# Kernel tuning notes

Hardware: AMD Instinct MI355X
Metric: run time of the kernel (lower is better)

The kernel has to match this reference:

```python
import jax, jax.numpy as jnp
import numpy as np

N_ATOMS = 8_000_000
N_REC = 2_000_000
N_POC = 500_000
N_CHAINS = 4


def setup_inputs() -> dict:
    key = jax.random.key(0)
    k1, k2, k3, k4 = jax.random.split(key, 4)
    # coordinates in nm, inside a ~5 nm box
    positions = jax.random.uniform(k1, (N_ATOMS, 3), dtype=jnp.float32) * 5.0
    box_vectors = jnp.diag(jnp.array([5.0, 5.0, 5.0], dtype=jnp.float32))
    # unique receptor atom indices into positions
    rec_indices = jax.random.permutation(k2, N_ATOMS)[:N_REC].astype(jnp.int32)
    # unique pocket indices INTO THE REC ARRAY (poc_pos = rec_pos[poc_indices])
    poc_indices = jax.random.permutation(k3, N_REC)[:N_POC].astype(jnp.int32)
    # contiguous chain assignment over rec atoms, all chains present in pocket
    chain_ids = ((jnp.arange(N_REC, dtype=jnp.int32) * N_CHAINS) // N_REC).astype(jnp.int32)
    poc_chain_ids = chain_ids[poc_indices]
    ref_poc = jax.random.uniform(k4, (N_POC, 3), dtype=jnp.float32) * 5.0
    k = jnp.float32(100.0)  # kJ/mol/nm^2
    return {
        "positions": positions, "box_vectors": box_vectors, "ref_poc": ref_poc,
        "k": k, "rec_indices": rec_indices, "poc_indices": poc_indices,
        "chain_ids": chain_ids, "poc_chain_ids": poc_chain_ids, "n_chains": N_CHAINS,
    }


def best_periodic_translation(pos1, pos2, box_vectors):
    # pos1, pos2: [C,3]; box_vectors: [3,3] (rows are lattice vectors)
    delta = pos2 - pos1
    inv = 1.0 / jnp.diag(box_vectors)
    s3 = jnp.round(delta[:, 2] * inv[2])
    delta = delta - s3[:, None] * box_vectors[2]
    s2 = jnp.round(delta[:, 1] * inv[1])
    delta = delta - s2[:, None] * box_vectors[1]
    s1 = jnp.round(delta[:, 0] * inv[0])
    return s1[:, None] * box_vectors[0] + s2[:, None] * box_vectors[1] + s3[:, None] * box_vectors[2]


def reference(positions, box_vectors, ref_poc, k, rec_indices, poc_indices, chain_ids, poc_chain_ids, n_chains):
    rec_pos = positions[rec_indices]  # [R,3]
    # Per-chain pocket COM. NOTE: original indexes global positions here
    # (positions[poc_chain_indices]), NOT rec_pos -- reproduced faithfully.
    poc_glob = positions[poc_indices]  # [P,3]
    counts = jax.ops.segment_sum(jnp.ones((poc_glob.shape[0],), poc_glob.dtype), poc_chain_ids, num_segments=n_chains)  # [C]
    poc_com = jax.ops.segment_sum(poc_glob, poc_chain_ids, num_segments=n_chains) / counts[:, None]  # [C,3]
    ref_com = jax.ops.segment_sum(ref_poc, poc_chain_ids, num_segments=n_chains) / counts[:, None]  # [C,3]
    best_t = best_periodic_translation(poc_com, ref_com, box_vectors)  # [C,3]
    rec_pos = rec_pos + best_t[chain_ids]  # translate each chain into the reference image

    poc_pos = rec_pos[poc_indices]  # [P,3]
    rec_origin = jnp.mean(rec_pos, axis=0)
    rec_centered = rec_pos - rec_origin
    r_sq = jnp.sum(rec_centered ** 2, axis=1)  # [R]
    F = jnp.zeros_like(rec_pos).at[poc_indices].set(-2.0 * k * (poc_pos - ref_poc))
    F_mean = jnp.mean(F, axis=0)
    torque = jnp.cross(rec_centered, F)
    torque_mean = jnp.mean(torque, axis=0)
    F_rot = jnp.cross(torque_mean[None], rec_centered) / r_sq[:, None]
    F_final = jnp.zeros_like(positions).at[rec_indices].set(F_mean + F_rot)
    return (jnp.float32(0.0), F_final)
```

## Files before the change

### kernel.cpp

```cpp
#include <hip/hip_runtime.h>


typedef unsigned int uint32;
typedef unsigned char uchar;

#define MAXC 16
#define W_BT 0
#define W_O 48
#define W_FM 52
#define W_TM 56
#define W_ACC 64

#define GCOUNT_OFF 4096
#define REC_OFF 8192
#define NB 512
#define BSH 14
#define BUCKET_ATOMS (1 << BSH)
#define CAP 5120
#define INV8_OFF (REC_OFF + NB * CAP * 4)

#define K1_KPT 16
#define K1_CHUNK (256 * K1_KPT)

__device__ inline float waveSum(float v) {
#pragma unroll
  for (int off = 32; off > 0; off >>= 1) v += __shfl_down(v, off, 64);
  return v;
}

__global__ __launch_bounds__(256) void k_part_pocket(
    const float* __restrict__ pos, const float* __restrict__ ref_poc,
    const int* __restrict__ rec_idx, const int* __restrict__ cid,
    const int* __restrict__ poc_idx, const int* __restrict__ poc_cid,
    const int* __restrict__ ncp, int R, int P,
    uint32* __restrict__ gcount, uint32* __restrict__ grecords,
    float* __restrict__ ws) {
  const int tid = threadIdx.x;
  const int C = ncp[0];
  const int gsz = gridDim.x * blockDim.x;

  if (C <= 4) {
    float vals[43];
#pragma unroll
    for (int v = 0; v < 43; ++v) vals[v] = 0.f;
    for (int r = blockIdx.x * blockDim.x + tid; r < P; r += gsz) {
      int i2 = poc_idx[r];
      int c2 = poc_cid[r];
      int ri = rec_idx[i2];
      float gx = pos[3 * i2 + 0], gy = pos[3 * i2 + 1], gz = pos[3 * i2 + 2];
      float px = pos[3 * ri + 0], py = pos[3 * ri + 1], pz = pos[3 * ri + 2];
      float rx = ref_poc[3 * r + 0], ry = ref_poc[3 * r + 1], rz = ref_poc[3 * r + 2];
      vals[0] += py * rz - pz * ry;
      vals[1] += pz * rx - px * rz;
      vals[2] += px * ry - py * rx;
#pragma unroll
      for (int cc = 0; cc < 4; ++cc) {
        bool m = (c2 == cc);
        float* a = &vals[3 + cc * 10];
        a[0] += m ? gx : 0.f;  a[1] += m ? gy : 0.f;  a[2] += m ? gz : 0.f;
        a[3] += m ? rx : 0.f;  a[4] += m ? ry : 0.f;  a[5] += m ? rz : 0.f;
        a[6] += m ? px : 0.f;  a[7] += m ? py : 0.f;  a[8] += m ? pz : 0.f;
        a[9] += m ? 1.f : 0.f;
      }
    }
    __shared__ float red[4][43];
    const int wid = tid >> 6;
#pragma unroll
    for (int v = 0; v < 43; ++v) {
      float s = waveSum(vals[v]);
      if ((tid & 63) == 0) red[wid][v] = s;
    }
    __syncthreads();
    for (int t = tid; t < 43; t += 256)
      atomicAdd(&ws[W_ACC + 19 + t],
                red[0][t] + red[1][t] + red[2][t] + red[3][t]);
    __syncthreads();
  } else {
    __shared__ float accL[3 + MAXC * 10];
    for (int t = tid; t < 3 + MAXC * 10; t += 256) accL[t] = 0.f;
    __syncthreads();
    for (int r = blockIdx.x * blockDim.x + tid; r < P; r += gsz) {
      int i2 = poc_idx[r];
      int c2 = poc_cid[r];
      int ri = rec_idx[i2];
      float gx = pos[3 * i2 + 0], gy = pos[3 * i2 + 1], gz = pos[3 * i2 + 2];
      float px = pos[3 * ri + 0], py = pos[3 * ri + 1], pz = pos[3 * ri + 2];
      float rx = ref_poc[3 * r + 0], ry = ref_poc[3 * r + 1], rz = ref_poc[3 * r + 2];
      atomicAdd(&accL[0], py * rz - pz * ry);
      atomicAdd(&accL[1], pz * rx - px * rz);
      atomicAdd(&accL[2], px * ry - py * rx);
      float* a = &accL[3 + c2 * 10];
      atomicAdd(&a[0], gx); atomicAdd(&a[1], gy); atomicAdd(&a[2], gz);
      atomicAdd(&a[3], rx); atomicAdd(&a[4], ry); atomicAdd(&a[5], rz);
      atomicAdd(&a[6], px); atomicAdd(&a[7], py); atomicAdd(&a[8], pz);
      atomicAdd(&a[9], 1.f);
    }
    __syncthreads();
    for (int t = tid; t < 3 + MAXC * 10; t += 256)
      if (accL[t] != 0.f) atomicAdd(&ws[W_ACC + 19 + t], accL[t]);
    __syncthreads();
  }

  __shared__ uint32 hist[NB], curs[NB], base[NB];
  for (int r0 = blockIdx.x * K1_CHUNK; r0 < R; r0 += gridDim.x * K1_CHUNK) {
    int cnt = R - r0; if (cnt > K1_CHUNK) cnt = K1_CHUNK;
    for (int t = tid; t < NB; t += 256) { hist[t] = 0u; curs[t] = 0u; }
    __syncthreads();
    uint32 enc[K1_KPT];
#pragma unroll
    for (int j = 0; j < K1_KPT; ++j) {
      int t = tid + j * 256;
      uint32 e = 0xFFFFFFFFu;
      if (t < cnt) {
        uint32 idx = (uint32)rec_idx[r0 + t];
        uint32 c = (uint32)cid[r0 + t] & 255u;
        e = (idx << 8) | c;
        atomicAdd(&hist[idx >> BSH], 1u);
      }
      enc[j] = e;
    }
    __syncthreads();
    for (int t = tid; t < NB; t += 256) {
      uint32 h = hist[t];
      base[t] = h ? atomicAdd(&gcount[t], h) : 0u;
    }
    __syncthreads();
#pragma unroll
    for (int j = 0; j < K1_KPT; ++j) {
      uint32 e = enc[j];
      if (e != 0xFFFFFFFFu) {
        uint32 b = e >> (8 + BSH);
        uint32 slot = base[b] + atomicAdd(&curs[b], 1u);
        if (slot < CAP) grecords[b * CAP + slot] = e;
      }
    }
    __syncthreads();
  }
}

__global__ __launch_bounds__(256) void k_bucket_build(
    const float4* __restrict__ pos4, const int* __restrict__ ncp,
    const uint32* __restrict__ gcount, const uint32* __restrict__ grecords,
    int N, uchar* __restrict__ inv8, float* __restrict__ ws) {
  const int tid = threadIdx.x;
  const int b = blockIdx.x;
  const int a0 = b << BSH;
  if (a0 >= N) return;
  int natoms = N - a0; if (natoms > BUCKET_ATOMS) natoms = BUCKET_ATOMS;

  __shared__ uchar map_[BUCKET_ATOMS];
  __shared__ float cnt16[MAXC];
  uint4* m16 = (uint4*)map_;
  uint4 ff; ff.x = ff.y = ff.z = ff.w = 0xFFFFFFFFu;
  for (int t = tid; t < BUCKET_ATOMS / 16; t += 256) m16[t] = ff;
  const int C = ncp[0];
  if (C > 4) for (int t = tid; t < MAXC; t += 256) cnt16[t] = 0.f;
  __syncthreads();

  int n = (int)gcount[b]; if (n > CAP) n = CAP;
  float c0 = 0.f, c1 = 0.f, c2 = 0.f, c3 = 0.f;
  for (int t = tid; t < n; t += 256) {
    uint32 e = grecords[b * CAP + t];
    uint32 ia = (e >> 8) & (BUCKET_ATOMS - 1);
    uint32 c = e & 255u;
    map_[ia] = (uchar)c;
    if (C <= 4) {
      c0 += (c == 0u) ? 1.f : 0.f;
      c1 += (c == 1u) ? 1.f : 0.f;
      c2 += (c == 2u) ? 1.f : 0.f;
      c3 += (c == 3u) ? 1.f : 0.f;
    } else {
      atomicAdd(&cnt16[c], 1.f);
    }
  }
  __syncthreads();

  uchar* dst = inv8 + a0;
  if (natoms == BUCKET_ATOMS) {
    uint4* d16 = (uint4*)dst;
    for (int t = tid; t < BUCKET_ATOMS / 16; t += 256) d16[t] = m16[t];
  } else {
    for (int t = tid; t < natoms; t += 256) dst[t] = map_[t];
  }

  float sx = 0.f, sy = 0.f, sz = 0.f;
  int ngf = natoms >> 2;
  const uchar4* m4 = (const uchar4*)map_;
  int g0 = a0 >> 2;
  for (int g = tid; g < ngf; g += 256) {
    float4 p0 = pos4[3 * (g0 + g) + 0];
    float4 p1 = pos4[3 * (g0 + g) + 1];
    float4 p2 = pos4[3 * (g0 + g) + 2];
    uchar4 m = m4[g];
    if (m.x != 255) { sx += p0.x; sy += p0.y; sz += p0.z; }
    if (m.y != 255) { sx += p0.w; sy += p1.x; sz += p1.y; }
    if (m.z != 255) { sx += p1.z; sy += p1.w; sz += p2.x; }
    if (m.w != 255) { sx += p2.y; sy += p2.z; sz += p2.w; }
  }
  int tb = natoms & 3;
  if (tid < tb) {
    int a = a0 + (ngf << 2) + tid;
    const float* pf = (const float*)pos4;
    if (map_[(ngf << 2) + tid] != 255) {
      sx += pf[3 * a]; sy += pf[3 * a + 1]; sz += pf[3 * a + 2];
    }
  }

  __shared__ float red[4][7];
  float vv[7] = {sx, sy, sz, c0, c1, c2, c3};
  const int wid = tid >> 6;
#pragma unroll
  for (int v = 0; v < 7; ++v) {
    float s = waveSum(vv[v]);
    if ((tid & 63) == 0) red[wid][v] = s;
  }
  __syncthreads();
  if (tid < 7) {
    float s = red[0][tid] + red[1][tid] + red[2][tid] + red[3][tid];
    atomicAdd(&ws[W_ACC + tid], s);
  }
  if (C > 4 && tid < C) atomicAdd(&ws[W_ACC + 3 + tid], cnt16[tid]);
}

__global__ void k_finalize(const float* __restrict__ box,
                           const float* __restrict__ kp,
                           const int* __restrict__ ncp,
                           int R, float* __restrict__ ws) {
  __shared__ float tot[192];
  const int C = ncp[0];
  for (int t = threadIdx.x; t < 192; t += blockDim.x) tot[t] = ws[W_ACC + t];
  __syncthreads();
  if (threadIdx.x != 0) return;
  const float kk = kp[0];
  const float Rf = (float)R;
  const float* xp = &tot[19];
  float inv0 = 1.f / box[0], inv1 = 1.f / box[4], inv2 = 1.f / box[8];
  float ox = tot[0], oy = tot[1], oz = tot[2];
  float Fx = 0, Fy = 0, Fz = 0;
  float T1x = 0, T1y = 0, T1z = 0, T2x = 0, T2y = 0, T2z = 0;
  for (int c = 0; c < C; ++c) {
    float nrec = tot[3 + c];
    const float* a = &tot[22 + c * 10];
    float np = a[9];
    float invn = 1.f / np;
    float pcx = a[0] * invn, pcy = a[1] * invn, pcz = a[2] * invn;
    float rcx = a[3] * invn, rcy = a[4] * invn, rcz = a[5] * invn;
    float dx = rcx - pcx, dy = rcy - pcy, dz = rcz - pcz;
    float s3 = rintf(dz * inv2);
    dx -= s3 * box[6]; dy -= s3 * box[7]; dz -= s3 * box[8];
    float s2 = rintf(dy * inv1);
    dx -= s2 * box[3]; dy -= s2 * box[4]; dz -= s2 * box[5];
    float s1 = rintf(dx * inv0);
    float btx = s1 * box[0] + s2 * box[3] + s3 * box[6];
    float bty = s1 * box[1] + s2 * box[4] + s3 * box[7];
    float btz = s1 * box[2] + s2 * box[5] + s3 * box[8];
    ws[W_BT + c * 3 + 0] = btx;
    ws[W_BT + c * 3 + 1] = bty;
    ws[W_BT + c * 3 + 2] = btz;
    ox += nrec * btx; oy += nrec * bty; oz += nrec * btz;
    float SFx = -2.f * kk * (a[6] + np * btx - a[3]);
    float SFy = -2.f * kk * (a[7] + np * bty - a[4]);
    float SFz = -2.f * kk * (a[8] + np * btz - a[5]);
    Fx += SFx; Fy += SFy; Fz += SFz;
    T1x += a[7] * btz - a[8] * bty;
    T1y += a[8] * btx - a[6] * btz;
    T1z += a[6] * bty - a[7] * btx;
    T2x += bty * SFz - btz * SFy;
    T2y += btz * SFx - btx * SFz;
    T2z += btx * SFy - bty * SFx;
  }
  ox /= Rf; oy /= Rf; oz /= Rf;
  float Tx = 2.f * kk * xp[0] - 2.f * kk * T1x + T2x - (oy * Fz - oz * Fy);
  float Ty = 2.f * kk * xp[1] - 2.f * kk * T1y + T2y - (oz * Fx - ox * Fz);
  float Tz = 2.f * kk * xp[2] - 2.f * kk * T1z + T2z - (ox * Fy - oy * Fx);
  ws[W_O + 0] = ox; ws[W_O + 1] = oy; ws[W_O + 2] = oz;
  ws[W_FM + 0] = Fx / Rf; ws[W_FM + 1] = Fy / Rf; ws[W_FM + 2] = Fz / Rf;
  ws[W_TM + 0] = Tx / Rf; ws[W_TM + 1] = Ty / Rf; ws[W_TM + 2] = Tz / Rf;
}

__global__ __launch_bounds__(256) void k_final_dense(
    const float* __restrict__ pos, const uchar* __restrict__ inv8,
    int N, const float* __restrict__ ws, float* __restrict__ out) {
  __shared__ float stage[3328];
  __shared__ float sc[64];
  const int tid = threadIdx.x;
  if (tid < 64) sc[tid] = ws[tid];
  const int t0 = blockIdx.x * 1024;
  int nat = N - t0; if (nat > 1024) nat = 1024;
  const int nfl = nat * 3;

  if (nat == 1024) {
    const float4* src4 = (const float4*)(pos + 3 * t0);
#pragma unroll
    for (int kk = 0; kk < 3; ++kk) {
      int v4 = tid + kk * 256;
      float4 p = src4[v4];
      int idx = 4 * v4 + v4 / 3;
      stage[idx + 0] = p.x; stage[idx + 1] = p.y;
      stage[idx + 2] = p.z; stage[idx + 3] = p.w;
    }
  } else {
    for (int k = tid; k < nfl; k += 256)
      stage[k + (int)((unsigned)k / 12u)] = pos[3 * t0 + k];
  }
  __syncthreads();

  float ox = sc[W_O + 0], oy = sc[W_O + 1], oz = sc[W_O + 2];
  float fmx = sc[W_FM + 0], fmy = sc[W_FM + 1], fmz = sc[W_FM + 2];
  float tmx = sc[W_TM + 0], tmy = sc[W_TM + 1], tmz = sc[W_TM + 2];

  uchar mc[4];
  if (nat == 1024) {
    uchar4 m = ((const uchar4*)(inv8 + t0))[tid];
    mc[0] = m.x; mc[1] = m.y; mc[2] = m.z; mc[3] = m.w;
  } else {
#pragma unroll
    for (int q = 0; q < 4; ++q) {
      int la = 4 * tid + q;
      mc[q] = (la < nat) ? inv8[t0 + la] : (uchar)255;
    }
  }
#pragma unroll
  for (int q = 0; q < 4; ++q) {
    int la = 4 * tid + q;
    if (la < nat) {
      float* s = &stage[13 * tid + 3 * q];
      float fx = 0.f, fy = 0.f, fz = 0.f;
      int c = mc[q];
      if (c != 255) {
        float cx = s[0] + sc[W_BT + 3 * c + 0] - ox;
        float cy = s[1] + sc[W_BT + 3 * c + 1] - oy;
        float cz = s[2] + sc[W_BT + 3 * c + 2] - oz;
        float inv = 1.f / (cx * cx + cy * cy + cz * cz);
        fx = fmx + (tmy * cz - tmz * cy) * inv;
        fy = fmy + (tmz * cx - tmx * cz) * inv;
        fz = fmz + (tmx * cy - tmy * cx) * inv;
      }
      s[0] = fx; s[1] = fy; s[2] = fz;
    }
  }
  __syncthreads();

  if (blockIdx.x == 0 && tid == 0) out[0] = 0.f;
  float* ob = out + 1 + 3 * t0;
  for (int k = tid; k < nfl; k += 256)
    ob[k] = stage[k + (int)((unsigned)k / 12u)];
}

extern "C" void kernel_launch(void* const* d_in, const int* in_sizes, int n_in,
                              void* d_out, int out_size, void* d_ws, size_t ws_size,
                              hipStream_t stream) {
  const float* pos     = (const float*)d_in[0];
  const float* box     = (const float*)d_in[1];
  const float* ref_poc = (const float*)d_in[2];
  const float* kp      = (const float*)d_in[3];
  const int* rec_idx   = (const int*)d_in[4];
  const int* poc_idx   = (const int*)d_in[5];
  const int* cid       = (const int*)d_in[6];
  const int* poc_cid   = (const int*)d_in[7];
  const int* ncp       = (const int*)d_in[8];
  float* out = (float*)d_out;
  float* ws  = (float*)d_ws;
  uint32* gcount   = (uint32*)((char*)d_ws + GCOUNT_OFF);
  uint32* grecords = (uint32*)((char*)d_ws + REC_OFF);
  uchar* inv8      = (uchar*)d_ws + INV8_OFF;

  const int N = in_sizes[0] / 3;
  const int R = in_sizes[4];
  const int P = in_sizes[5];

  hipMemsetAsync(d_ws, 0, 8192, stream);

  k_part_pocket<<<1024, 256, 0, stream>>>(pos, ref_poc, rec_idx, cid, poc_idx,
                                          poc_cid, ncp, R, P, gcount, grecords, ws);
  k_bucket_build<<<NB, 256, 0, stream>>>((const float4*)pos, ncp, gcount,
                                         grecords, N, inv8, ws);
  k_finalize<<<1, 256, 0, stream>>>(box, kp, ncp, R, ws);
  int gF = (N + 1023) / 1024;
  k_final_dense<<<gF, 256, 0, stream>>>(pos, inv8, N, ws, out);
}
```

Measured before the change: 280.9 us.

## Split first kernel into dedicated pocket and partition blocks, vectorize output stores

The first kernel now runs two disjoint block groups: 512 blocks do the pocket reduction while another 512 blocks do the receptor bucket partition, so the two jobs run concurrently instead of every block doing both in sequence. The pocket loop handles four elements per thread with the loads issued in batches to expose more memory-level parallelism, and shared memory is overlaid through a union. The final dense kernel writes full 1024-atom tiles with aligned float4 stores instead of scalar stores. The trade-offs are a possibly unbalanced split between the two block groups and more registers used in the batched pocket loop.

```diff
diff --git a/kernel.cpp b/kernel.cpp
--- a/kernel.cpp
+++ b/kernel.cpp
@@ -19,16 +19,22 @@
 #define CAP 5120
 #define INV8_OFF (REC_OFF + NB * CAP * 4)
 
+#define PB 512
+#define RB 512
 #define K1_KPT 16
 #define K1_CHUNK (256 * K1_KPT)
 
+struct PartSh { uint32 hist[NB]; uint32 curs[NB]; uint32 base[NB]; };
+struct PocSh  { float red[4][43]; float accL[3 + MAXC * 10]; };
+union ShU { PartSh part; PocSh poc; };
+
 __device__ inline float waveSum(float v) {
 #pragma unroll
   for (int off = 32; off > 0; off >>= 1) v += __shfl_down(v, off, 64);
   return v;
 }
 
-__global__ __launch_bounds__(256) void k_part_pocket(
+__global__ __launch_bounds__(256) void k_fused(
     const float* __restrict__ pos, const float* __restrict__ ref_poc,
     const int* __restrict__ rec_idx, const int* __restrict__ cid,
     const int* __restrict__ poc_idx, const int* __restrict__ poc_cid,
@@ -36,105 +42,141 @@
     uint32* __restrict__ gcount, uint32* __restrict__ grecords,
     float* __restrict__ ws) {
   const int tid = threadIdx.x;
+  const int bid = blockIdx.x;
+  __shared__ ShU sh;
   const int C = ncp[0];
-  const int gsz = gridDim.x * blockDim.x;
-
-  if (C <= 4) {
-    float vals[43];
-#pragma unroll
-    for (int v = 0; v < 43; ++v) vals[v] = 0.f;
-    for (int r = blockIdx.x * blockDim.x + tid; r < P; r += gsz) {
-      int i2 = poc_idx[r];
-      int c2 = poc_cid[r];
-      int ri = rec_idx[i2];
-      float gx = pos[3 * i2 + 0], gy = pos[3 * i2 + 1], gz = pos[3 * i2 + 2];
-      float px = pos[3 * ri + 0], py = pos[3 * ri + 1], pz = pos[3 * ri + 2];
-      float rx = ref_poc[3 * r + 0], ry = ref_poc[3 * r + 1], rz = ref_poc[3 * r + 2];
-      vals[0] += py * rz - pz * ry;
-      vals[1] += pz * rx - px * rz;
-      vals[2] += px * ry - py * rx;
-#pragma unroll
-      for (int cc = 0; cc < 4; ++cc) {
-        bool m = (c2 == cc);
-        float* a = &vals[3 + cc * 10];
-        a[0] += m ? gx : 0.f;  a[1] += m ? gy : 0.f;  a[2] += m ? gz : 0.f;
-        a[3] += m ? rx : 0.f;  a[4] += m ? ry : 0.f;  a[5] += m ? rz : 0.f;
-        a[6] += m ? px : 0.f;  a[7] += m ? py : 0.f;  a[8] += m ? pz : 0.f;
-        a[9] += m ? 1.f : 0.f;
-      }
-    }
-    __shared__ float red[4][43];
-    const int wid = tid >> 6;
-#pragma unroll
-    for (int v = 0; v < 43; ++v) {
-      float s = waveSum(vals[v]);
-      if ((tid & 63) == 0) red[wid][v] = s;
-    }
-    __syncthreads();
-    for (int t = tid; t < 43; t += 256)
-      atomicAdd(&ws[W_ACC + 19 + t],
-                red[0][t] + red[1][t] + red[2][t] + red[3][t]);
-    __syncthreads();
+
+  if (bid < PB) {
+    const int gsz = PB * 256;
+    if (C <= 4) {
+      float vals[43];
+#pragma unroll
+      for (int v = 0; v < 43; ++v) vals[v] = 0.f;
+      for (int rb = bid * 256 + tid; rb < P; rb += 4 * gsz) {
+        int rr[4], i2[4], c2[4], ri[4];
+        float g[4][3], p[4][3], rf[4][3];
+#pragma unroll
+        for (int q = 0; q < 4; ++q) {
+          int r = rb + q * gsz;
+          rr[q] = (r < P) ? r : -1;
+        }
+#pragma unroll
+        for (int q = 0; q < 4; ++q) {
+          int r = (rr[q] < 0) ? 0 : rr[q];
+          i2[q] = poc_idx[r];
+          c2[q] = poc_cid[r];
+        }
+#pragma unroll
+        for (int q = 0; q < 4; ++q) {
+          ri[q] = rec_idx[i2[q]];
+          g[q][0] = pos[3 * i2[q] + 0];
+          g[q][1] = pos[3 * i2[q] + 1];
+          g[q][2] = pos[3 * i2[q] + 2];
+        }
+#pragma unroll
+        for (int q = 0; q < 4; ++q) {
+          int r = (rr[q] < 0) ? 0 : rr[q];
+          p[q][0] = pos[3 * ri[q] + 0];
+          p[q][1] = pos[3 * ri[q] + 1];
+          p[q][2] = pos[3 * ri[q] + 2];
+          rf[q][0] = ref_poc[3 * r + 0];
+          rf[q][1] = ref_poc[3 * r + 1];
+          rf[q][2] = ref_poc[3 * r + 2];
+        }
+#pragma unroll
+        for (int q = 0; q < 4; ++q) {
+          if (rr[q] >= 0) {
+            vals[0] += p[q][1] * rf[q][2] - p[q][2] * rf[q][1];
+            vals[1] += p[q][2] * rf[q][0] - p[q][0] * rf[q][2];
+            vals[2] += p[q][0] * rf[q][1] - p[q][1] * rf[q][0];
+#pragma unroll
+            for (int cc = 0; cc < 4; ++cc) {
+              bool m = (c2[q] == cc);
+              float* a = &vals[3 + cc * 10];
+              a[0] += m ? g[q][0] : 0.f; a[1] += m ? g[q][1] : 0.f;
+              a[2] += m ? g[q][2] : 0.f;
+              a[3] += m ? rf[q][0] : 0.f; a[4] += m ? rf[q][1] : 0.f;
+              a[5] += m ? rf[q][2] : 0.f;
+              a[6] += m ? p[q][0] : 0.f; a[7] += m ? p[q][1] : 0.f;
+              a[8] += m ? p[q][2] : 0.f;
+              a[9] += m ? 1.f : 0.f;
+            }
+          }
+        }
+      }
+      const int wid = tid >> 6;
+#pragma unroll
+      for (int v = 0; v < 43; ++v) {
+        float s = waveSum(vals[v]);
+        if ((tid & 63) == 0) sh.poc.red[wid][v] = s;
+      }
+      __syncthreads();
+      for (int t = tid; t < 43; t += 256)
+        atomicAdd(&ws[W_ACC + 19 + t], sh.poc.red[0][t] + sh.poc.red[1][t] +
+                                       sh.poc.red[2][t] + sh.poc.red[3][t]);
+    } else {
+      float* accL = sh.poc.accL;
+      for (int t = tid; t < 3 + MAXC * 10; t += 256) accL[t] = 0.f;
+      __syncthreads();
+      for (int r = bid * 256 + tid; r < P; r += PB * 256) {
+        int i2 = poc_idx[r];
+        int c2 = poc_cid[r];
+        int ri = rec_idx[i2];
+        float gx = pos[3 * i2 + 0], gy = pos[3 * i2 + 1], gz = pos[3 * i2 + 2];
+        float px = pos[3 * ri + 0], py = pos[3 * ri + 1], pz = pos[3 * ri + 2];
+        float rx = ref_poc[3 * r + 0], ry = ref_poc[3 * r + 1], rz = ref_poc[3 * r + 2];
+        atomicAdd(&accL[0], py * rz - pz * ry);
+        atomicAdd(&accL[1], pz * rx - px * rz);
+        atomicAdd(&accL[2], px * ry - py * rx);
+        float* a = &accL[3 + c2 * 10];
+        atomicAdd(&a[0], gx); atomicAdd(&a[1], gy); atomicAdd(&a[2], gz);
+        atomicAdd(&a[3], rx); atomicAdd(&a[4], ry); atomicAdd(&a[5], rz);
+        atomicAdd(&a[6], px); atomicAdd(&a[7], py); atomicAdd(&a[8], pz);
+        atomicAdd(&a[9], 1.f);
+      }
+      __syncthreads();
+      for (int t = tid; t < 3 + MAXC * 10; t += 256)
+        if (accL[t] != 0.f) atomicAdd(&ws[W_ACC + 19 + t], accL[t]);
+    }
   } else {
-    __shared__ float accL[3 + MAXC * 10];
-    for (int t = tid; t < 3 + MAXC * 10; t += 256) accL[t] = 0.f;
-    __syncthreads();
-    for (int r = blockIdx.x * blockDim.x + tid; r < P; r += gsz) {
-      int i2 = poc_idx[r];
-      int c2 = poc_cid[r];
-      int ri = rec_idx[i2];
-      float gx = pos[3 * i2 + 0], gy = pos[3 * i2 + 1], gz = pos[3 * i2 + 2];
-      float px = pos[3 * ri + 0], py = pos[3 * ri + 1], pz = pos[3 * ri + 2];
-      float rx = ref_poc[3 * r + 0], ry = ref_poc[3 * r + 1], rz = ref_poc[3 * r + 2];
-      atomicAdd(&accL[0], py * rz - pz * ry);
-      atomicAdd(&accL[1], pz * rx - px * rz);
-      atomicAdd(&accL[2], px * ry - py * rx);
-      float* a = &accL[3 + c2 * 10];
-      atomicAdd(&a[0], gx); atomicAdd(&a[1], gy); atomicAdd(&a[2], gz);
-      atomicAdd(&a[3], rx); atomicAdd(&a[4], ry); atomicAdd(&a[5], rz);
-      atomicAdd(&a[6], px); atomicAdd(&a[7], py); atomicAdd(&a[8], pz);
-      atomicAdd(&a[9], 1.f);
-    }
-    __syncthreads();
-    for (int t = tid; t < 3 + MAXC * 10; t += 256)
-      if (accL[t] != 0.f) atomicAdd(&ws[W_ACC + 19 + t], accL[t]);
-    __syncthreads();
-  }
-
-  __shared__ uint32 hist[NB], curs[NB], base[NB];
-  for (int r0 = blockIdx.x * K1_CHUNK; r0 < R; r0 += gridDim.x * K1_CHUNK) {
-    int cnt = R - r0; if (cnt > K1_CHUNK) cnt = K1_CHUNK;
-    for (int t = tid; t < NB; t += 256) { hist[t] = 0u; curs[t] = 0u; }
-    __syncthreads();
-    uint32 enc[K1_KPT];
-#pragma unroll
-    for (int j = 0; j < K1_KPT; ++j) {
-      int t = tid + j * 256;
-      uint32 e = 0xFFFFFFFFu;
-      if (t < cnt) {
-        uint32 idx = (uint32)rec_idx[r0 + t];
-        uint32 c = (uint32)cid[r0 + t] & 255u;
-        e = (idx << 8) | c;
-        atomicAdd(&hist[idx >> BSH], 1u);
-      }
-      enc[j] = e;
-    }
-    __syncthreads();
-    for (int t = tid; t < NB; t += 256) {
-      uint32 h = hist[t];
-      base[t] = h ? atomicAdd(&gcount[t], h) : 0u;
-    }
-    __syncthreads();
-#pragma unroll
-    for (int j = 0; j < K1_KPT; ++j) {
-      uint32 e = enc[j];
-      if (e != 0xFFFFFFFFu) {
-        uint32 b = e >> (8 + BSH);
-        uint32 slot = base[b] + atomicAdd(&curs[b], 1u);
-        if (slot < CAP) grecords[b * CAP + slot] = e;
-      }
-    }
-    __syncthreads();
+    const int pb = bid - PB;
+    uint32* hist = sh.part.hist;
+    uint32* curs = sh.part.curs;
+    uint32* base = sh.part.base;
+    for (int r0 = pb * K1_CHUNK; r0 < R; r0 += RB * K1_CHUNK) {
+      int cnt = R - r0; if (cnt > K1_CHUNK) cnt = K1_CHUNK;
+      for (int t = tid; t < NB; t += 256) { hist[t] = 0u; curs[t] = 0u; }
+      __syncthreads();
+      uint32 enc[K1_KPT];
+#pragma unroll
+      for (int j = 0; j < K1_KPT; ++j) {
+        int t = tid + j * 256;
+        uint32 e = 0xFFFFFFFFu;
+        if (t < cnt) {
+          uint32 idx = (uint32)rec_idx[r0 + t];
+          uint32 c = (uint32)cid[r0 + t] & 255u;
+          e = (idx << 8) | c;
+          atomicAdd(&hist[idx >> BSH], 1u);
+        }
+        enc[j] = e;
+      }
+      __syncthreads();
+      for (int t = tid; t < NB; t += 256) {
+        uint32 h = hist[t];
+        base[t] = h ? atomicAdd(&gcount[t], h) : 0u;
+      }
+      __syncthreads();
+#pragma unroll
+      for (int j = 0; j < K1_KPT; ++j) {
+        uint32 e = enc[j];
+        if (e != 0xFFFFFFFFu) {
+          uint32 b = e >> (8 + BSH);
+          uint32 slot = base[b] + atomicAdd(&curs[b], 1u);
+          if (slot < CAP) grecords[b * CAP + slot] = e;
+        }
+      }
+      __syncthreads();
+    }
   }
 }
 
@@ -343,8 +385,26 @@
 
   if (blockIdx.x == 0 && tid == 0) out[0] = 0.f;
   float* ob = out + 1 + 3 * t0;
-  for (int k = tid; k < nfl; k += 256)
-    ob[k] = stage[k + (int)((unsigned)k / 12u)];
+  if (nat == 1024) {
+#pragma unroll
+    for (int kk = 0; kk < 3; ++kk) {
+      int j = tid + kk * 256;
+      if (j < 767) {
+        int k = 3 + 4 * j;
+        float4 v;
+        v.x = stage[k + k / 12];
+        v.y = stage[(k + 1) + (k + 1) / 12];
+        v.z = stage[(k + 2) + (k + 2) / 12];
+        v.w = stage[(k + 3) + (k + 3) / 12];
+        *(float4*)(ob + k) = v;
+      }
+    }
+    if (tid < 3) ob[tid] = stage[tid];
+    if (tid == 3) ob[3071] = stage[3071 + 3071 / 12];
+  } else {
+    for (int k = tid; k < nfl; k += 256)
+      ob[k] = stage[k + (int)((unsigned)k / 12u)];
+  }
 }
 
 extern "C" void kernel_launch(void* const* d_in, const int* in_sizes, int n_in,
@@ -371,8 +431,8 @@
 
   hipMemsetAsync(d_ws, 0, 8192, stream);
 
-  k_part_pocket<<<1024, 256, 0, stream>>>(pos, ref_poc, rec_idx, cid, poc_idx,
-                                          poc_cid, ncp, R, P, gcount, grecords, ws);
+  k_fused<<<PB + RB, 256, 0, stream>>>(pos, ref_poc, rec_idx, cid, poc_idx,
+                                       poc_cid, ncp, R, P, gcount, grecords, ws);
   k_bucket_build<<<NB, 256, 0, stream>>>((const float4*)pos, ncp, gcount,
                                          grecords, N, inv8, ws);
   k_finalize<<<1, 256, 0, stream>>>(box, kp, ncp, R, ws);
```

After: 267.6 us. 4.8% less time.
